# Kernel tuning notes

Measured on AMD Instinct MI355X. Metric: run time of the kernel, lower is better.

Reference implementation:

```python
import jax, jax.numpy as jnp
import numpy as np

N_NODES = 100000
N_EDGES = 3200000
F_IN = 128
H = 32
C = 8


def _graph_conv(x, src, dst, ew, W_rel, b_rel, W_root):
    # PyG GraphConv: sum-aggregate edge_weight * x[src] into dst, then
    # lin_rel(agg) + lin_root(x). lin_root has no bias.
    msg = x[src] * ew[:, None]                                  # [E, F]
    agg = jax.ops.segment_sum(msg, dst, num_segments=N_NODES)   # [N, F]
    return agg @ W_rel.T + b_rel + x @ W_root.T


def setup_inputs() -> dict:
    key = jax.random.key(0)
    ks = jax.random.split(key, 12)
    x = jax.random.normal(ks[0], (N_NODES, F_IN), dtype=jnp.float32)
    edge_index = jax.random.randint(ks[1], (2, N_EDGES), 0, N_NODES, dtype=jnp.int32)
    edge_weights = jax.random.uniform(ks[2], (N_EDGES,), dtype=jnp.float32)
    s = lambda fan_in: 1.0 / np.sqrt(fan_in)
    W1_rel = jax.random.uniform(ks[3], (H, F_IN), minval=-s(F_IN), maxval=s(F_IN), dtype=jnp.float32)
    b1 = jax.random.uniform(ks[4], (H,), minval=-s(F_IN), maxval=s(F_IN), dtype=jnp.float32)
    W1_root = jax.random.uniform(ks[5], (H, F_IN), minval=-s(F_IN), maxval=s(F_IN), dtype=jnp.float32)
    W2_rel = jax.random.uniform(ks[6], (H, H), minval=-s(H), maxval=s(H), dtype=jnp.float32)
    b2 = jax.random.uniform(ks[7], (H,), minval=-s(H), maxval=s(H), dtype=jnp.float32)
    W2_root = jax.random.uniform(ks[8], (H, H), minval=-s(H), maxval=s(H), dtype=jnp.float32)
    W3_rel = jax.random.uniform(ks[9], (C, H), minval=-s(H), maxval=s(H), dtype=jnp.float32)
    b3 = jax.random.uniform(ks[10], (C,), minval=-s(H), maxval=s(H), dtype=jnp.float32)
    W3_root = jax.random.uniform(ks[11], (C, H), minval=-s(H), maxval=s(H), dtype=jnp.float32)
    return {"x": x, "edge_index": edge_index, "edge_weights": edge_weights,
            "W1_rel": W1_rel, "b1": b1, "W1_root": W1_root,
            "W2_rel": W2_rel, "b2": b2, "W2_root": W2_root,
            "W3_rel": W3_rel, "b3": b3, "W3_root": W3_root}


def reference(x, edge_index, edge_weights,
              W1_rel, b1, W1_root, W2_rel, b2, W2_root, W3_rel, b3, W3_root):
    src, dst = edge_index[0], edge_index[1]
    h = _graph_conv(x, src, dst, edge_weights, W1_rel, b1, W1_root)
    h = jax.nn.leaky_relu(h, negative_slope=0.01)
    # dropout is identity in eval mode
    h = _graph_conv(h, src, dst, edge_weights, W2_rel, b2, W2_root)
    h = jax.nn.leaky_relu(h, negative_slope=0.01)
    out = _graph_conv(h, src, dst, edge_weights, W3_rel, b3, W3_root)
    return out
```

## Files before the change

### kernel.cpp

```cpp
#include <hip/hip_runtime.h>

#define NN 100000
#define NE 3200000
#define FIN 128
#define HD 32
#define CD 8
#define NPB 256
#define NBUCK ((NN + NPB - 1) / NPB)
#define CHUNK_B 8192

typedef unsigned int uint;

__device__ __forceinline__ float lrelu(float v) { return v > 0.f ? v : 0.01f * v; }
__device__ __forceinline__ uint bf16rne(float x) {
    uint u = __float_as_uint(x);
    return (u + 0x7FFFu + ((u >> 16) & 1u)) >> 16;
}
__device__ __forceinline__ uint pack2(float a, float b) {
    return bf16rne(a) | (bf16rne(b) << 16);
}
__device__ __forceinline__ float lo16(uint v) { return __uint_as_float(v << 16); }
__device__ __forceinline__ float hi16(uint v) { return __uint_as_float(v & 0xFFFF0000u); }


__global__ __launch_bounds__(256) void k_proj128(
    const float* __restrict__ x, const float* __restrict__ Wrel,
    const float* __restrict__ Wroot, const float* __restrict__ b,
    uint* __restrict__ pB, float* __restrict__ R)
{
    __shared__ float Wt[FIN][64];
    for (int idx = threadIdx.x; idx < FIN * 64; idx += 256) {
        int k = idx >> 6, j = idx & 63;
        Wt[k][j] = (j < HD) ? Wrel[j * FIN + k] : Wroot[(j - HD) * FIN + k];
    }
    __syncthreads();
    int n = blockIdx.x * 256 + threadIdx.x;
    if (n >= NN) return;

    float accP[HD], accR[HD];
#pragma unroll
    for (int j = 0; j < HD; ++j) { accP[j] = 0.f; accR[j] = 0.f; }

    const float4* x4 = (const float4*)(x + (size_t)n * FIN);
#pragma unroll 2
    for (int k4 = 0; k4 < FIN / 4; ++k4) {
        float4 xv = x4[k4];
        float xs[4] = {xv.x, xv.y, xv.z, xv.w};
#pragma unroll
        for (int kk = 0; kk < 4; ++kk) {
            float xk = xs[kk];
            int k = k4 * 4 + kk;
#pragma unroll
            for (int j = 0; j < HD; ++j) {
                accP[j] += xk * Wt[k][j];
                accR[j] += xk * Wt[k][j + HD];
            }
        }
    }
    uint4* pp = (uint4*)(pB + (size_t)n * 16);
#pragma unroll
    for (int q = 0; q < 4; ++q)
        pp[q] = make_uint4(pack2(accP[8*q+0], accP[8*q+1]), pack2(accP[8*q+2], accP[8*q+3]),
                           pack2(accP[8*q+4], accP[8*q+5]), pack2(accP[8*q+6], accP[8*q+7]));
    float4* rr = (float4*)(R + (size_t)n * HD);
#pragma unroll
    for (int q = 0; q < HD / 4; ++q)
        rr[q] = make_float4(accR[4*q+0] + b[4*q+0], accR[4*q+1] + b[4*q+1],
                            accR[4*q+2] + b[4*q+2], accR[4*q+3] + b[4*q+3]);
}

__global__ __launch_bounds__(256) void k_mid(
    const float* __restrict__ G, const float* R_in,
    const float* __restrict__ Wrel, const float* __restrict__ Wroot,
    const float* __restrict__ b,
    uint* __restrict__ pB, float* R_out)
{
    __shared__ float Ws[HD][64];
    for (int idx = threadIdx.x; idx < HD * 64; idx += 256) {
        int k = idx >> 6, j = idx & 63;
        Ws[k][j] = (j < HD) ? Wrel[j * HD + k] : Wroot[(j - HD) * HD + k];
    }
    __syncthreads();
    int n = blockIdx.x * 256 + threadIdx.x;
    if (n >= NN) return;

    float h[HD];
    const float4* av = (const float4*)(G + (size_t)n * HD);
    const float4* rv = (const float4*)(R_in + (size_t)n * HD);
#pragma unroll
    for (int q = 0; q < HD / 4; ++q) {
        float4 a = av[q], r_ = rv[q];
        h[4*q+0] = lrelu(a.x + r_.x);
        h[4*q+1] = lrelu(a.y + r_.y);
        h[4*q+2] = lrelu(a.z + r_.z);
        h[4*q+3] = lrelu(a.w + r_.w);
    }
    float accP[HD], accR[HD];
#pragma unroll
    for (int j = 0; j < HD; ++j) { accP[j] = 0.f; accR[j] = 0.f; }
#pragma unroll 4
    for (int k = 0; k < HD; ++k) {
        float hk = h[k];
#pragma unroll
        for (int j = 0; j < HD; ++j) {
            accP[j] += hk * Ws[k][j];
            accR[j] += hk * Ws[k][j + HD];
        }
    }
    uint4* pp = (uint4*)(pB + (size_t)n * 16);
#pragma unroll
    for (int q = 0; q < 4; ++q)
        pp[q] = make_uint4(pack2(accP[8*q+0], accP[8*q+1]), pack2(accP[8*q+2], accP[8*q+3]),
                           pack2(accP[8*q+4], accP[8*q+5]), pack2(accP[8*q+6], accP[8*q+7]));
    float4* rr = (float4*)(R_out + (size_t)n * HD);
#pragma unroll
    for (int q = 0; q < HD / 4; ++q)
        rr[q] = make_float4(accR[4*q+0] + b[4*q+0], accR[4*q+1] + b[4*q+1],
                            accR[4*q+2] + b[4*q+2], accR[4*q+3] + b[4*q+3]);
}

__global__ __launch_bounds__(256) void k_last(
    const float* __restrict__ G, const float* __restrict__ R,
    const float* __restrict__ Wrel, const float* __restrict__ Wroot,
    const float* __restrict__ b,
    uint* __restrict__ p3B, float* __restrict__ out)
{
    __shared__ float Ws[HD][16];
    for (int idx = threadIdx.x; idx < HD * 16; idx += 256) {
        int k = idx >> 4, j = idx & 15;
        Ws[k][j] = (j < CD) ? Wrel[j * HD + k] : Wroot[(j - CD) * HD + k];
    }
    __syncthreads();
    int n = blockIdx.x * 256 + threadIdx.x;
    if (n >= NN) return;

    float h[HD];
    const float4* av = (const float4*)(G + (size_t)n * HD);
    const float4* rv = (const float4*)(R + (size_t)n * HD);
#pragma unroll
    for (int q = 0; q < HD / 4; ++q) {
        float4 a = av[q], r_ = rv[q];
        h[4*q+0] = lrelu(a.x + r_.x);
        h[4*q+1] = lrelu(a.y + r_.y);
        h[4*q+2] = lrelu(a.z + r_.z);
        h[4*q+3] = lrelu(a.w + r_.w);
    }
    float accP[CD], accR[CD];
#pragma unroll
    for (int j = 0; j < CD; ++j) { accP[j] = 0.f; accR[j] = 0.f; }
#pragma unroll
    for (int k = 0; k < HD; ++k) {
        float hk = h[k];
#pragma unroll
        for (int j = 0; j < CD; ++j) {
            accP[j] += hk * Ws[k][j];
            accR[j] += hk * Ws[k][j + CD];
        }
    }
    uint4* pp = (uint4*)(p3B + (size_t)n * 4);
    pp[0] = make_uint4(pack2(accP[0], accP[1]), pack2(accP[2], accP[3]),
                       pack2(accP[4], accP[5]), pack2(accP[6], accP[7]));
    float4* oo = (float4*)(out + (size_t)n * CD);
    oo[0] = make_float4(accR[0] + b[0], accR[1] + b[1], accR[2] + b[2], accR[3] + b[3]);
    oo[1] = make_float4(accR[4] + b[4], accR[5] + b[5], accR[6] + b[6], accR[7] + b[7]);
}


__global__ __launch_bounds__(256) void k_bhist(
    const int* __restrict__ dst, int* __restrict__ bcnt)
{
    __shared__ int lc[NBUCK];
    int t = threadIdx.x;
    for (int i = t; i < NBUCK; i += 256) lc[i] = 0;
    __syncthreads();
    for (int e = blockIdx.x * 256 + t; e < NE; e += gridDim.x * 256)
        atomicAdd(&lc[dst[e] >> 8], 1);
    __syncthreads();
    for (int i = t; i < NBUCK; i += 256) {
        int c = lc[i];
        if (c) atomicAdd(&bcnt[i], c);
    }
}

__global__ __launch_bounds__(512) void k_bscan(
    const int* __restrict__ bcnt, int* __restrict__ bbase, int* __restrict__ bcur)
{
    __shared__ int s[512];
    int t = threadIdx.x;
    s[t] = (t < NBUCK) ? bcnt[t] : 0;
    __syncthreads();
    for (int off = 1; off < 512; off <<= 1) {
        int a = (t >= off) ? s[t - off] : 0;
        __syncthreads();
        s[t] += a;
        __syncthreads();
    }
    int excl = t ? s[t - 1] : 0;
    if (t < NBUCK) { bbase[t] = excl; bcur[t] = excl; }
    if (t == 0) bbase[NBUCK] = NE;
}

__global__ __launch_bounds__(256) void k_bscatter(
    const int* __restrict__ src, const int* __restrict__ dst, const float* __restrict__ ew,
    int* __restrict__ bcur, int2* __restrict__ tmp)
{
    __shared__ int lc[NBUCK];
    int t = threadIdx.x;
    for (int i = t; i < NBUCK; i += 256) lc[i] = 0;
    __syncthreads();
    int base = blockIdx.x * CHUNK_B;
#pragma unroll 4
    for (int k = 0; k < CHUNK_B / 256; ++k) {
        int e = base + k * 256 + t;
        if (e < NE) atomicAdd(&lc[dst[e] >> 8], 1);
    }
    __syncthreads();
    for (int b = t; b < NBUCK; b += 256) {
        int c = lc[b];
        lc[b] = c ? atomicAdd(&bcur[b], c) : 0;
    }
    __syncthreads();
#pragma unroll 4
    for (int k = 0; k < CHUNK_B / 256; ++k) {
        int e = base + k * 256 + t;
        if (e < NE) {
            int d = dst[e];
            int pos = atomicAdd(&lc[d >> 8], 1);
            tmp[pos] = make_int2(src[e] | ((d & 255) << 17), __float_as_int(ew[e]));
        }
    }
}

__global__ __launch_bounds__(256) void k_bsort(
    const int* __restrict__ bbase, const int2* __restrict__ tmp,
    int2* __restrict__ epack, int* __restrict__ rowstart)
{
    int b = blockIdx.x, t = threadIdx.x;
    int lo = bbase[b], hi = bbase[b + 1], cnt = hi - lo;
    __shared__ int hist[NPB];
    __shared__ int sc[NPB];
    __shared__ int cur[NPB];
    hist[t] = 0;
    __syncthreads();
    for (int i = t; i < cnt; i += 256)
        atomicAdd(&hist[(tmp[lo + i].x >> 17) & 255], 1);
    __syncthreads();
    sc[t] = hist[t];
    __syncthreads();
    for (int off = 1; off < 256; off <<= 1) {
        int a = (t >= off) ? sc[t - off] : 0;
        __syncthreads();
        sc[t] += a;
        __syncthreads();
    }
    int excl = t ? sc[t - 1] : 0;
    int node = (b << 8) + t;
    if (node < NN) rowstart[node] = lo + excl;
    if (b == 0 && t == 0) rowstart[NN] = NE;
    cur[t] = lo + excl;
    __syncthreads();
    for (int i = t; i < cnt; i += 256) {
        int2 v = tmp[lo + i];
        int l = (v.x >> 17) & 255;
        int pos = atomicAdd(&cur[l], 1);
        epack[pos] = make_int2(v.x & 0x1FFFF, v.y);
    }
}


__global__ __launch_bounds__(256) void k_gather32(
    const int* __restrict__ rowstart, const int2* __restrict__ epack,
    const uint* __restrict__ pB, float* __restrict__ G)
{
    int wid = (blockIdx.x * 256 + threadIdx.x) >> 6;
    if (wid >= NN) return;
    int lane = threadIdx.x & 63;
    int q = lane >> 4, f2 = lane & 15;
    int rs = rowstart[wid], re = rowstart[wid + 1];

    float a0 = 0.f, a1 = 0.f, b0 = 0.f, b1 = 0.f;
    int e = rs + q;
    for (; e + 4 < re; e += 8) {
        int2 p0 = epack[e];
        int2 p1 = epack[e + 4];
        uint v0 = pB[((size_t)p0.x << 4) + f2];
        uint v1 = pB[((size_t)p1.x << 4) + f2];
        float w0 = __int_as_float(p0.y), w1 = __int_as_float(p1.y);
        a0 += lo16(v0) * w0; a1 += hi16(v0) * w0;
        b0 += lo16(v1) * w1; b1 += hi16(v1) * w1;
    }
    for (; e < re; e += 4) {
        int2 p0 = epack[e];
        uint v0 = pB[((size_t)p0.x << 4) + f2];
        float w0 = __int_as_float(p0.y);
        a0 += lo16(v0) * w0; a1 += hi16(v0) * w0;
    }
    a0 += b0; a1 += b1;
    a0 += __shfl_xor(a0, 16); a1 += __shfl_xor(a1, 16);
    a0 += __shfl_xor(a0, 32); a1 += __shfl_xor(a1, 32);
    if (lane < 16) {
        float2* g2 = (float2*)(G + (size_t)wid * HD + 2 * f2);
        *g2 = make_float2(a0, a1);
    }
}

__global__ __launch_bounds__(256) void k_gather8(
    const int* __restrict__ rowstart, const int2* __restrict__ epack,
    const uint* __restrict__ p3B, float* __restrict__ out)
{
    int wid = (blockIdx.x * 256 + threadIdx.x) >> 6;
    if (wid >= NN) return;
    int lane = threadIdx.x & 63;
    int q = lane >> 2, f2 = lane & 3;
    int rs = rowstart[wid], re = rowstart[wid + 1];

    float a0 = 0.f, a1 = 0.f, b0 = 0.f, b1 = 0.f;
    int e = rs + q;
    for (; e + 16 < re; e += 32) {
        int2 p0 = epack[e];
        int2 p1 = epack[e + 16];
        uint v0 = p3B[((size_t)p0.x << 2) + f2];
        uint v1 = p3B[((size_t)p1.x << 2) + f2];
        float w0 = __int_as_float(p0.y), w1 = __int_as_float(p1.y);
        a0 += lo16(v0) * w0; a1 += hi16(v0) * w0;
        b0 += lo16(v1) * w1; b1 += hi16(v1) * w1;
    }
    for (; e < re; e += 16) {
        int2 p0 = epack[e];
        uint v0 = p3B[((size_t)p0.x << 2) + f2];
        float w0 = __int_as_float(p0.y);
        a0 += lo16(v0) * w0; a1 += hi16(v0) * w0;
    }
    a0 += b0; a1 += b1;
    a0 += __shfl_xor(a0, 4);  a1 += __shfl_xor(a1, 4);
    a0 += __shfl_xor(a0, 8);  a1 += __shfl_xor(a1, 8);
    a0 += __shfl_xor(a0, 16); a1 += __shfl_xor(a1, 16);
    a0 += __shfl_xor(a0, 32); a1 += __shfl_xor(a1, 32);
    if (lane < 4) {
        float2* o2 = (float2*)(out + (size_t)wid * CD + 2 * f2);
        float2 t = *o2;
        t.x += a0; t.y += a1;
        *o2 = t;
    }
}


extern "C" void kernel_launch(void* const* d_in, const int* in_sizes, int n_in,
                              void* d_out, int out_size, void* d_ws, size_t ws_size,
                              hipStream_t stream)
{
    const float* x      = (const float*)d_in[0];
    const int*   ei     = (const int*)d_in[1];
    const float* ew     = (const float*)d_in[2];
    const float* W1rel  = (const float*)d_in[3];
    const float* b1     = (const float*)d_in[4];
    const float* W1root = (const float*)d_in[5];
    const float* W2rel  = (const float*)d_in[6];
    const float* b2     = (const float*)d_in[7];
    const float* W2root = (const float*)d_in[8];
    const float* W3rel  = (const float*)d_in[9];
    const float* b3     = (const float*)d_in[10];
    const float* W3root = (const float*)d_in[11];
    float* out = (float*)d_out;

    const int* src = ei;
    const int* dst = ei + NE;

    char* ws = (char*)d_ws;
    int2*  epack    = (int2*)ws;   ws += (size_t)NE * sizeof(int2);
    char*  unionA   = ws;          ws += (size_t)NE * sizeof(int2);
    uint*  pB       = (uint*)ws;   ws += (size_t)NN * 16 * 4;
    uint*  p3B      = (uint*)ws;   ws += (size_t)NN * 4 * 4;
    int*   rowstart = (int*)ws;    ws += (size_t)(NN + 1) * 4;
    int*   bcnt     = (int*)ws;    ws += (size_t)NBUCK * 4;
    int*   bbase    = (int*)ws;    ws += (size_t)(NBUCK + 1) * 4;
    int*   bcur     = (int*)ws;

    int2*  tmp = (int2*)unionA;
    float* G   = (float*)unionA;
    float* R   = G + (size_t)NN * HD;

    const int nodeBlocks = (NN + 255) / 256;
    const int waveBlocks = (NN + 3) / 4;
    const int scatBlocks = (NE + CHUNK_B - 1) / CHUNK_B;

    hipMemsetAsync(bcnt, 0, (size_t)NBUCK * 4, stream);
    k_bhist<<<512, 256, 0, stream>>>(dst, bcnt);
    k_bscan<<<1, 512, 0, stream>>>(bcnt, bbase, bcur);
    k_bscatter<<<scatBlocks, 256, 0, stream>>>(src, dst, ew, bcur, tmp);
    k_bsort<<<NBUCK, 256, 0, stream>>>(bbase, tmp, epack, rowstart);

    k_proj128<<<nodeBlocks, 256, 0, stream>>>(x, W1rel, W1root, b1, pB, R);
    k_gather32<<<waveBlocks, 256, 0, stream>>>(rowstart, epack, pB, G);
    k_mid<<<nodeBlocks, 256, 0, stream>>>(G, R, W2rel, W2root, b2, pB, R);
    k_gather32<<<waveBlocks, 256, 0, stream>>>(rowstart, epack, pB, G);
    k_last<<<nodeBlocks, 256, 0, stream>>>(G, R, W3rel, W3root, b3, p3B, out);
    k_gather8<<<waveBlocks, 256, 0, stream>>>(rowstart, epack, p3B, out);
}
```

Before: 484.9 us.

## Fuse per-node projections into gather kernels and vectorize edge bucketing loads

Merges the mid and last per-node projection kernels into the gather kernels. Each wave aggregates its node, applies leaky-relu with the root term, stores the hidden vector in shared memory and computes the next layer's projections per lane. This removes two kernel launches and the global round trip of the aggregated G buffer, but needs separate pB1/pB2 buffers and a block-wide sync after the gather. The histogram and scatter kernels are also changed to read int4/float4 vectors with 512-thread blocks, the sort kernel moves to 512 threads, and the gather loop is unrolled by three instead of two.

```diff
diff --git a/kernel.cpp b/kernel.cpp
--- a/kernel.cpp
+++ b/kernel.cpp
@@ -2,6 +2,7 @@
 
 #define NN 100000
 #define NE 3200000
+#define NE4 (NE / 4)
 #define FIN 128
 #define HD 32
 #define CD 8
@@ -69,114 +70,24 @@
                             accR[4*q+2] + b[4*q+2], accR[4*q+3] + b[4*q+3]);
 }
 
-__global__ __launch_bounds__(256) void k_mid(
-    const float* __restrict__ G, const float* R_in,
-    const float* __restrict__ Wrel, const float* __restrict__ Wroot,
-    const float* __restrict__ b,
-    uint* __restrict__ pB, float* R_out)
-{
-    __shared__ float Ws[HD][64];
-    for (int idx = threadIdx.x; idx < HD * 64; idx += 256) {
-        int k = idx >> 6, j = idx & 63;
-        Ws[k][j] = (j < HD) ? Wrel[j * HD + k] : Wroot[(j - HD) * HD + k];
-    }
-    __syncthreads();
-    int n = blockIdx.x * 256 + threadIdx.x;
-    if (n >= NN) return;
-
-    float h[HD];
-    const float4* av = (const float4*)(G + (size_t)n * HD);
-    const float4* rv = (const float4*)(R_in + (size_t)n * HD);
-#pragma unroll
-    for (int q = 0; q < HD / 4; ++q) {
-        float4 a = av[q], r_ = rv[q];
-        h[4*q+0] = lrelu(a.x + r_.x);
-        h[4*q+1] = lrelu(a.y + r_.y);
-        h[4*q+2] = lrelu(a.z + r_.z);
-        h[4*q+3] = lrelu(a.w + r_.w);
-    }
-    float accP[HD], accR[HD];
-#pragma unroll
-    for (int j = 0; j < HD; ++j) { accP[j] = 0.f; accR[j] = 0.f; }
-#pragma unroll 4
-    for (int k = 0; k < HD; ++k) {
-        float hk = h[k];
-#pragma unroll
-        for (int j = 0; j < HD; ++j) {
-            accP[j] += hk * Ws[k][j];
-            accR[j] += hk * Ws[k][j + HD];
-        }
-    }
-    uint4* pp = (uint4*)(pB + (size_t)n * 16);
-#pragma unroll
-    for (int q = 0; q < 4; ++q)
-        pp[q] = make_uint4(pack2(accP[8*q+0], accP[8*q+1]), pack2(accP[8*q+2], accP[8*q+3]),
-                           pack2(accP[8*q+4], accP[8*q+5]), pack2(accP[8*q+6], accP[8*q+7]));
-    float4* rr = (float4*)(R_out + (size_t)n * HD);
-#pragma unroll
-    for (int q = 0; q < HD / 4; ++q)
-        rr[q] = make_float4(accR[4*q+0] + b[4*q+0], accR[4*q+1] + b[4*q+1],
-                            accR[4*q+2] + b[4*q+2], accR[4*q+3] + b[4*q+3]);
-}
-
-__global__ __launch_bounds__(256) void k_last(
-    const float* __restrict__ G, const float* __restrict__ R,
-    const float* __restrict__ Wrel, const float* __restrict__ Wroot,
-    const float* __restrict__ b,
-    uint* __restrict__ p3B, float* __restrict__ out)
-{
-    __shared__ float Ws[HD][16];
-    for (int idx = threadIdx.x; idx < HD * 16; idx += 256) {
-        int k = idx >> 4, j = idx & 15;
-        Ws[k][j] = (j < CD) ? Wrel[j * HD + k] : Wroot[(j - CD) * HD + k];
-    }
-    __syncthreads();
-    int n = blockIdx.x * 256 + threadIdx.x;
-    if (n >= NN) return;
-
-    float h[HD];
-    const float4* av = (const float4*)(G + (size_t)n * HD);
-    const float4* rv = (const float4*)(R + (size_t)n * HD);
-#pragma unroll
-    for (int q = 0; q < HD / 4; ++q) {
-        float4 a = av[q], r_ = rv[q];
-        h[4*q+0] = lrelu(a.x + r_.x);
-        h[4*q+1] = lrelu(a.y + r_.y);
-        h[4*q+2] = lrelu(a.z + r_.z);
-        h[4*q+3] = lrelu(a.w + r_.w);
-    }
-    float accP[CD], accR[CD];
-#pragma unroll
-    for (int j = 0; j < CD; ++j) { accP[j] = 0.f; accR[j] = 0.f; }
-#pragma unroll
-    for (int k = 0; k < HD; ++k) {
-        float hk = h[k];
-#pragma unroll
-        for (int j = 0; j < CD; ++j) {
-            accP[j] += hk * Ws[k][j];
-            accR[j] += hk * Ws[k][j + CD];
-        }
-    }
-    uint4* pp = (uint4*)(p3B + (size_t)n * 4);
-    pp[0] = make_uint4(pack2(accP[0], accP[1]), pack2(accP[2], accP[3]),
-                       pack2(accP[4], accP[5]), pack2(accP[6], accP[7]));
-    float4* oo = (float4*)(out + (size_t)n * CD);
-    oo[0] = make_float4(accR[0] + b[0], accR[1] + b[1], accR[2] + b[2], accR[3] + b[3]);
-    oo[1] = make_float4(accR[4] + b[4], accR[5] + b[5], accR[6] + b[6], accR[7] + b[7]);
-}
-
-
-__global__ __launch_bounds__(256) void k_bhist(
+
+__global__ __launch_bounds__(512) void k_bhist(
     const int* __restrict__ dst, int* __restrict__ bcnt)
 {
     __shared__ int lc[NBUCK];
     int t = threadIdx.x;
-    for (int i = t; i < NBUCK; i += 256) lc[i] = 0;
-    __syncthreads();
-    for (int e = blockIdx.x * 256 + t; e < NE; e += gridDim.x * 256)
-        atomicAdd(&lc[dst[e] >> 8], 1);
-    __syncthreads();
-    for (int i = t; i < NBUCK; i += 256) {
+    for (int i = t; i < NBUCK; i += 512) lc[i] = 0;
+    __syncthreads();
+    const int4* dst4 = (const int4*)dst;
+    for (int i4 = blockIdx.x * 512 + t; i4 < NE4; i4 += gridDim.x * 512) {
+        int4 d = dst4[i4];
+        atomicAdd(&lc[d.x >> 8], 1);
+        atomicAdd(&lc[d.y >> 8], 1);
+        atomicAdd(&lc[d.z >> 8], 1);
+        atomicAdd(&lc[d.w >> 8], 1);
+    }
+    __syncthreads();
+    for (int i = t; i < NBUCK; i += 512) {
         int c = lc[i];
         if (c) atomicAdd(&bcnt[i], c);
     }
@@ -200,38 +111,52 @@
     if (t == 0) bbase[NBUCK] = NE;
 }
 
-__global__ __launch_bounds__(256) void k_bscatter(
+__global__ __launch_bounds__(512) void k_bscatter(
     const int* __restrict__ src, const int* __restrict__ dst, const float* __restrict__ ew,
     int* __restrict__ bcur, int2* __restrict__ tmp)
 {
     __shared__ int lc[NBUCK];
     int t = threadIdx.x;
-    for (int i = t; i < NBUCK; i += 256) lc[i] = 0;
-    __syncthreads();
-    int base = blockIdx.x * CHUNK_B;
-#pragma unroll 4
-    for (int k = 0; k < CHUNK_B / 256; ++k) {
-        int e = base + k * 256 + t;
-        if (e < NE) atomicAdd(&lc[dst[e] >> 8], 1);
-    }
-    __syncthreads();
-    for (int b = t; b < NBUCK; b += 256) {
+    for (int i = t; i < NBUCK; i += 512) lc[i] = 0;
+    __syncthreads();
+    const int4* dst4 = (const int4*)dst;
+    const int4* src4 = (const int4*)src;
+    const float4* ew4 = (const float4*)ew;
+    int base4 = blockIdx.x * (CHUNK_B / 4);
+#pragma unroll
+    for (int k = 0; k < CHUNK_B / 4 / 512; ++k) {
+        int i4 = base4 + k * 512 + t;
+        if (i4 < NE4) {
+            int4 d = dst4[i4];
+            atomicAdd(&lc[d.x >> 8], 1);
+            atomicAdd(&lc[d.y >> 8], 1);
+            atomicAdd(&lc[d.z >> 8], 1);
+            atomicAdd(&lc[d.w >> 8], 1);
+        }
+    }
+    __syncthreads();
+    for (int b = t; b < NBUCK; b += 512) {
         int c = lc[b];
         lc[b] = c ? atomicAdd(&bcur[b], c) : 0;
     }
     __syncthreads();
-#pragma unroll 4
-    for (int k = 0; k < CHUNK_B / 256; ++k) {
-        int e = base + k * 256 + t;
-        if (e < NE) {
-            int d = dst[e];
-            int pos = atomicAdd(&lc[d >> 8], 1);
-            tmp[pos] = make_int2(src[e] | ((d & 255) << 17), __float_as_int(ew[e]));
+#pragma unroll
+    for (int k = 0; k < CHUNK_B / 4 / 512; ++k) {
+        int i4 = base4 + k * 512 + t;
+        if (i4 < NE4) {
+            int4 d = dst4[i4];
+            int4 s = src4[i4];
+            float4 w = ew4[i4];
+            int pos;
+            pos = atomicAdd(&lc[d.x >> 8], 1); tmp[pos] = make_int2(s.x | ((d.x & 255) << 17), __float_as_int(w.x));
+            pos = atomicAdd(&lc[d.y >> 8], 1); tmp[pos] = make_int2(s.y | ((d.y & 255) << 17), __float_as_int(w.y));
+            pos = atomicAdd(&lc[d.z >> 8], 1); tmp[pos] = make_int2(s.z | ((d.z & 255) << 17), __float_as_int(w.z));
+            pos = atomicAdd(&lc[d.w >> 8], 1); tmp[pos] = make_int2(s.w | ((d.w & 255) << 17), __float_as_int(w.w));
         }
     }
 }
 
-__global__ __launch_bounds__(256) void k_bsort(
+__global__ __launch_bounds__(512) void k_bsort(
     const int* __restrict__ bbase, const int2* __restrict__ tmp,
     int2* __restrict__ epack, int* __restrict__ rowstart)
 {
@@ -240,26 +165,28 @@
     __shared__ int hist[NPB];
     __shared__ int sc[NPB];
     __shared__ int cur[NPB];
-    hist[t] = 0;
-    __syncthreads();
-    for (int i = t; i < cnt; i += 256)
+    if (t < NPB) hist[t] = 0;
+    __syncthreads();
+    for (int i = t; i < cnt; i += 512)
         atomicAdd(&hist[(tmp[lo + i].x >> 17) & 255], 1);
     __syncthreads();
-    sc[t] = hist[t];
-    __syncthreads();
-    for (int off = 1; off < 256; off <<= 1) {
-        int a = (t >= off) ? sc[t - off] : 0;
+    if (t < NPB) sc[t] = hist[t];
+    __syncthreads();
+    for (int off = 1; off < NPB; off <<= 1) {
+        int a = (t < NPB && t >= off) ? sc[t - off] : 0;
         __syncthreads();
-        sc[t] += a;
+        if (t < NPB) sc[t] += a;
         __syncthreads();
     }
-    int excl = t ? sc[t - 1] : 0;
-    int node = (b << 8) + t;
-    if (node < NN) rowstart[node] = lo + excl;
+    if (t < NPB) {
+        int excl = t ? sc[t - 1] : 0;
+        int node = (b << 8) + t;
+        if (node < NN) rowstart[node] = lo + excl;
+        cur[t] = lo + excl;
+    }
     if (b == 0 && t == 0) rowstart[NN] = NE;
-    cur[t] = lo + excl;
-    __syncthreads();
-    for (int i = t; i < cnt; i += 256) {
+    __syncthreads();
+    for (int i = t; i < cnt; i += 512) {
         int2 v = tmp[lo + i];
         int l = (v.x >> 17) & 255;
         int pos = atomicAdd(&cur[l], 1);
@@ -268,39 +195,125 @@
 }
 
 
-__global__ __launch_bounds__(256) void k_gather32(
+__global__ __launch_bounds__(256) void k_gatherMid(
     const int* __restrict__ rowstart, const int2* __restrict__ epack,
-    const uint* __restrict__ pB, float* __restrict__ G)
-{
+    const uint* __restrict__ pB1, float* R,
+    const float* __restrict__ Wrel, const float* __restrict__ Wroot,
+    const float* __restrict__ b2, uint* __restrict__ pB2)
+{
+    __shared__ float Ws[HD][64];
+    __shared__ float hS[4][HD];
+    for (int idx = threadIdx.x; idx < HD * 64; idx += 256) {
+        int k = idx >> 6, j = idx & 63;
+        Ws[k][j] = (j < HD) ? Wrel[j * HD + k] : Wroot[(j - HD) * HD + k];
+    }
     int wid = (blockIdx.x * 256 + threadIdx.x) >> 6;
-    if (wid >= NN) return;
     int lane = threadIdx.x & 63;
+    int w = threadIdx.x >> 6;
     int q = lane >> 4, f2 = lane & 15;
     int rs = rowstart[wid], re = rowstart[wid + 1];
 
-    float a0 = 0.f, a1 = 0.f, b0 = 0.f, b1 = 0.f;
+    float a0 = 0.f, a1 = 0.f, c0 = 0.f, c1 = 0.f, d0 = 0.f, d1 = 0.f;
     int e = rs + q;
-    for (; e + 4 < re; e += 8) {
+    for (; e + 8 < re; e += 12) {
         int2 p0 = epack[e];
         int2 p1 = epack[e + 4];
-        uint v0 = pB[((size_t)p0.x << 4) + f2];
-        uint v1 = pB[((size_t)p1.x << 4) + f2];
-        float w0 = __int_as_float(p0.y), w1 = __int_as_float(p1.y);
-        a0 += lo16(v0) * w0; a1 += hi16(v0) * w0;
-        b0 += lo16(v1) * w1; b1 += hi16(v1) * w1;
+        int2 p2 = epack[e + 8];
+        uint v0 = pB1[((size_t)p0.x << 4) + f2];
+        uint v1 = pB1[((size_t)p1.x << 4) + f2];
+        uint v2 = pB1[((size_t)p2.x << 4) + f2];
+        float w0 = __int_as_float(p0.y), w1 = __int_as_float(p1.y), w2 = __int_as_float(p2.y);
+        a0 += lo16(v0) * w0; a1 += hi16(v0) * w0;
+        c0 += lo16(v1) * w1; c1 += hi16(v1) * w1;
+        d0 += lo16(v2) * w2; d1 += hi16(v2) * w2;
     }
     for (; e < re; e += 4) {
         int2 p0 = epack[e];
-        uint v0 = pB[((size_t)p0.x << 4) + f2];
+        uint v0 = pB1[((size_t)p0.x << 4) + f2];
         float w0 = __int_as_float(p0.y);
         a0 += lo16(v0) * w0; a1 += hi16(v0) * w0;
     }
-    a0 += b0; a1 += b1;
+    a0 += c0 + d0; a1 += c1 + d1;
     a0 += __shfl_xor(a0, 16); a1 += __shfl_xor(a1, 16);
     a0 += __shfl_xor(a0, 32); a1 += __shfl_xor(a1, 32);
     if (lane < 16) {
-        float2* g2 = (float2*)(G + (size_t)wid * HD + 2 * f2);
-        *g2 = make_float2(a0, a1);
+        float2 rv = *(const float2*)(R + (size_t)wid * HD + 2 * f2);
+        float2 hv = make_float2(lrelu(a0 + rv.x), lrelu(a1 + rv.y));
+        *(float2*)&hS[w][2 * f2] = hv;
+    }
+    __syncthreads();
+
+    int j = lane;
+    float acc = 0.f;
+#pragma unroll 8
+    for (int k = 0; k < HD; ++k) acc += hS[w][k] * Ws[k][j];
+    float other = __shfl_xor(acc, 1);
+    if (j < HD) {
+        if (!(j & 1)) pB2[(size_t)wid * 16 + (j >> 1)] = pack2(acc, other);
+    } else {
+        R[(size_t)wid * HD + (j - HD)] = acc + b2[j - HD];
+    }
+}
+
+__global__ __launch_bounds__(256) void k_gatherLast(
+    const int* __restrict__ rowstart, const int2* __restrict__ epack,
+    const uint* __restrict__ pB2, const float* __restrict__ R,
+    const float* __restrict__ Wrel, const float* __restrict__ Wroot,
+    const float* __restrict__ b3, uint* __restrict__ p3B, float* __restrict__ out)
+{
+    __shared__ float Ws[HD][16];
+    __shared__ float hS[4][HD];
+    for (int idx = threadIdx.x; idx < HD * 16; idx += 256) {
+        int k = idx >> 4, j = idx & 15;
+        Ws[k][j] = (j < CD) ? Wrel[j * HD + k] : Wroot[(j - CD) * HD + k];
+    }
+    int wid = (blockIdx.x * 256 + threadIdx.x) >> 6;
+    int lane = threadIdx.x & 63;
+    int w = threadIdx.x >> 6;
+    int q = lane >> 4, f2 = lane & 15;
+    int rs = rowstart[wid], re = rowstart[wid + 1];
+
+    float a0 = 0.f, a1 = 0.f, c0 = 0.f, c1 = 0.f, d0 = 0.f, d1 = 0.f;
+    int e = rs + q;
+    for (; e + 8 < re; e += 12) {
+        int2 p0 = epack[e];
+        int2 p1 = epack[e + 4];
+        int2 p2 = epack[e + 8];
+        uint v0 = pB2[((size_t)p0.x << 4) + f2];
+        uint v1 = pB2[((size_t)p1.x << 4) + f2];
+        uint v2 = pB2[((size_t)p2.x << 4) + f2];
+        float w0 = __int_as_float(p0.y), w1 = __int_as_float(p1.y), w2 = __int_as_float(p2.y);
+        a0 += lo16(v0) * w0; a1 += hi16(v0) * w0;
+        c0 += lo16(v1) * w1; c1 += hi16(v1) * w1;
+        d0 += lo16(v2) * w2; d1 += hi16(v2) * w2;
+    }
+    for (; e < re; e += 4) {
+        int2 p0 = epack[e];
+        uint v0 = pB2[((size_t)p0.x << 4) + f2];
+        float w0 = __int_as_float(p0.y);
+        a0 += lo16(v0) * w0; a1 += hi16(v0) * w0;
+    }
+    a0 += c0 + d0; a1 += c1 + d1;
+    a0 += __shfl_xor(a0, 16); a1 += __shfl_xor(a1, 16);
+    a0 += __shfl_xor(a0, 32); a1 += __shfl_xor(a1, 32);
+    if (lane < 16) {
+        float2 rv = *(const float2*)(R + (size_t)wid * HD + 2 * f2);
+        float2 hv = make_float2(lrelu(a0 + rv.x), lrelu(a1 + rv.y));
+        *(float2*)&hS[w][2 * f2] = hv;
+    }
+    __syncthreads();
+
+    if (lane < 16) {
+        int j = lane;
+        float acc = 0.f;
+#pragma unroll 8
+        for (int k = 0; k < HD; ++k) acc += hS[w][k] * Ws[k][j];
+        float other = __shfl_xor(acc, 1);
+        if (j < CD) {
+            if (!(j & 1)) p3B[(size_t)wid * 4 + (j >> 1)] = pack2(acc, other);
+        } else {
+            out[(size_t)wid * CD + (j - CD)] = acc + b3[j - CD];
+        }
     }
 }
 
@@ -368,32 +381,28 @@
 
     char* ws = (char*)d_ws;
     int2*  epack    = (int2*)ws;   ws += (size_t)NE * sizeof(int2);
-    char*  unionA   = ws;          ws += (size_t)NE * sizeof(int2);
-    uint*  pB       = (uint*)ws;   ws += (size_t)NN * 16 * 4;
+    int2*  tmp      = (int2*)ws;   ws += (size_t)NE * sizeof(int2);
+    float* R        = (float*)ws;  ws += (size_t)NN * HD * 4;
+    uint*  pB1      = (uint*)ws;   ws += (size_t)NN * 16 * 4;
+    uint*  pB2      = (uint*)ws;   ws += (size_t)NN * 16 * 4;
     uint*  p3B      = (uint*)ws;   ws += (size_t)NN * 4 * 4;
     int*   rowstart = (int*)ws;    ws += (size_t)(NN + 1) * 4;
     int*   bcnt     = (int*)ws;    ws += (size_t)NBUCK * 4;
     int*   bbase    = (int*)ws;    ws += (size_t)(NBUCK + 1) * 4;
     int*   bcur     = (int*)ws;
 
-    int2*  tmp = (int2*)unionA;
-    float* G   = (float*)unionA;
-    float* R   = G + (size_t)NN * HD;
-
     const int nodeBlocks = (NN + 255) / 256;
     const int waveBlocks = (NN + 3) / 4;
     const int scatBlocks = (NE + CHUNK_B - 1) / CHUNK_B;
 
     hipMemsetAsync(bcnt, 0, (size_t)NBUCK * 4, stream);
-    k_bhist<<<512, 256, 0, stream>>>(dst, bcnt);
+    k_bhist<<<512, 512, 0, stream>>>(dst, bcnt);
     k_bscan<<<1, 512, 0, stream>>>(bcnt, bbase, bcur);
-    k_bscatter<<<scatBlocks, 256, 0, stream>>>(src, dst, ew, bcur, tmp);
-    k_bsort<<<NBUCK, 256, 0, stream>>>(bbase, tmp, epack, rowstart);
-
-    k_proj128<<<nodeBlocks, 256, 0, stream>>>(x, W1rel, W1root, b1, pB, R);
-    k_gather32<<<waveBlocks, 256, 0, stream>>>(rowstart, epack, pB, G);
-    k_mid<<<nodeBlocks, 256, 0, stream>>>(G, R, W2rel, W2root, b2, pB, R);
-    k_gather32<<<waveBlocks, 256, 0, stream>>>(rowstart, epack, pB, G);
-    k_last<<<nodeBlocks, 256, 0, stream>>>(G, R, W3rel, W3root, b3, p3B, out);
+    k_bscatter<<<scatBlocks, 512, 0, stream>>>(src, dst, ew, bcur, tmp);
+    k_bsort<<<NBUCK, 512, 0, stream>>>(bbase, tmp, epack, rowstart);
+
+    k_proj128<<<nodeBlocks, 256, 0, stream>>>(x, W1rel, W1root, b1, pB1, R);
+    k_gatherMid<<<waveBlocks, 256, 0, stream>>>(rowstart, epack, pB1, R, W2rel, W2root, b2, pB2);
+    k_gatherLast<<<waveBlocks, 256, 0, stream>>>(rowstart, epack, pB2, R, W3rel, W3root, b3, p3B, out);
     k_gather8<<<waveBlocks, 256, 0, stream>>>(rowstart, epack, p3B, out);
 }
```

New measurement: 525.5 us. 1.08x slower.

## Locally sort bucket scatter in shared memory for coalesced writes; widen sort kernels

Applied to the files above, without the earlier changes.

The bucket scatter kernel now builds a per-chunk permutation in shared memory. It scans the local histogram so that edges of the same bucket are written to contiguous global positions, instead of each edge being scattered on its own through a shared atomic. The histogram kernel reads dst four at a time as int4, and the three sort-phase kernels move to 512-thread blocks. The aim is more coalesced global writes and fewer memory transactions in the CSR build. The cost is extra shared-memory use, an added 512-wide scan, and a second read of dst per chunk.

```diff
diff --git a/kernel.cpp b/kernel.cpp
--- a/kernel.cpp
+++ b/kernel.cpp
@@ -2,6 +2,7 @@
 
 #define NN 100000
 #define NE 3200000
+#define NE4 (NE / 4)
 #define FIN 128
 #define HD 32
 #define CD 8
@@ -10,6 +11,7 @@
 #define CHUNK_B 8192
 
 typedef unsigned int uint;
+typedef unsigned short ushort;
 
 __device__ __forceinline__ float lrelu(float v) { return v > 0.f ? v : 0.01f * v; }
 __device__ __forceinline__ uint bf16rne(float x) {
@@ -68,6 +70,7 @@
         rr[q] = make_float4(accR[4*q+0] + b[4*q+0], accR[4*q+1] + b[4*q+1],
                             accR[4*q+2] + b[4*q+2], accR[4*q+3] + b[4*q+3]);
 }
+
 
 __global__ __launch_bounds__(256) void k_mid(
     const float* __restrict__ G, const float* R_in,
@@ -166,17 +169,23 @@
 }
 
 
-__global__ __launch_bounds__(256) void k_bhist(
+__global__ __launch_bounds__(512) void k_bhist(
     const int* __restrict__ dst, int* __restrict__ bcnt)
 {
     __shared__ int lc[NBUCK];
     int t = threadIdx.x;
-    for (int i = t; i < NBUCK; i += 256) lc[i] = 0;
-    __syncthreads();
-    for (int e = blockIdx.x * 256 + t; e < NE; e += gridDim.x * 256)
-        atomicAdd(&lc[dst[e] >> 8], 1);
-    __syncthreads();
-    for (int i = t; i < NBUCK; i += 256) {
+    for (int i = t; i < NBUCK; i += 512) lc[i] = 0;
+    __syncthreads();
+    const int4* dst4 = (const int4*)dst;
+    for (int i4 = blockIdx.x * 512 + t; i4 < NE4; i4 += gridDim.x * 512) {
+        int4 d = dst4[i4];
+        atomicAdd(&lc[d.x >> 8], 1);
+        atomicAdd(&lc[d.y >> 8], 1);
+        atomicAdd(&lc[d.z >> 8], 1);
+        atomicAdd(&lc[d.w >> 8], 1);
+    }
+    __syncthreads();
+    for (int i = t; i < NBUCK; i += 512) {
         int c = lc[i];
         if (c) atomicAdd(&bcnt[i], c);
     }
@@ -200,38 +209,54 @@
     if (t == 0) bbase[NBUCK] = NE;
 }
 
-__global__ __launch_bounds__(256) void k_bscatter(
+__global__ __launch_bounds__(512) void k_bscatter(
     const int* __restrict__ src, const int* __restrict__ dst, const float* __restrict__ ew,
     int* __restrict__ bcur, int2* __restrict__ tmp)
 {
-    __shared__ int lc[NBUCK];
+    __shared__ int hist[NBUCK];
+    __shared__ int s[512];
+    __shared__ int off[NBUCK];
+    __shared__ int cur[NBUCK];
+    __shared__ ushort perm[CHUNK_B];
     int t = threadIdx.x;
-    for (int i = t; i < NBUCK; i += 256) lc[i] = 0;
-    __syncthreads();
     int base = blockIdx.x * CHUNK_B;
-#pragma unroll 4
-    for (int k = 0; k < CHUNK_B / 256; ++k) {
-        int e = base + k * 256 + t;
-        if (e < NE) atomicAdd(&lc[dst[e] >> 8], 1);
-    }
-    __syncthreads();
-    for (int b = t; b < NBUCK; b += 256) {
-        int c = lc[b];
-        lc[b] = c ? atomicAdd(&bcur[b], c) : 0;
-    }
-    __syncthreads();
-#pragma unroll 4
-    for (int k = 0; k < CHUNK_B / 256; ++k) {
-        int e = base + k * 256 + t;
-        if (e < NE) {
-            int d = dst[e];
-            int pos = atomicAdd(&lc[d >> 8], 1);
-            tmp[pos] = make_int2(src[e] | ((d & 255) << 17), __float_as_int(ew[e]));
-        }
-    }
-}
-
-__global__ __launch_bounds__(256) void k_bsort(
+    int cnt = min(CHUNK_B, NE - base);
+
+    for (int i = t; i < NBUCK; i += 512) hist[i] = 0;
+    __syncthreads();
+    for (int i = t; i < cnt; i += 512)
+        atomicAdd(&hist[dst[base + i] >> 8], 1);
+    __syncthreads();
+    s[t] = (t < NBUCK) ? hist[t] : 0;
+    __syncthreads();
+    for (int o = 1; o < 512; o <<= 1) {
+        int a = (t >= o) ? s[t - o] : 0;
+        __syncthreads();
+        s[t] += a;
+        __syncthreads();
+    }
+    if (t < NBUCK) {
+        int excl = t ? s[t - 1] : 0;
+        int c = hist[t];
+        int g = c ? atomicAdd(&bcur[t], c) : 0;
+        off[t] = g - excl;
+        cur[t] = excl;
+    }
+    __syncthreads();
+    for (int i = t; i < cnt; i += 512) {
+        int b = dst[base + i] >> 8;
+        int r = atomicAdd(&cur[b], 1);
+        perm[r] = (ushort)i;
+    }
+    __syncthreads();
+    for (int i = t; i < cnt; i += 512) {
+        int e = base + (int)perm[i];
+        int d = dst[e];
+        tmp[off[d >> 8] + i] = make_int2(src[e] | ((d & 255) << 17), __float_as_int(ew[e]));
+    }
+}
+
+__global__ __launch_bounds__(512) void k_bsort(
     const int* __restrict__ bbase, const int2* __restrict__ tmp,
     int2* __restrict__ epack, int* __restrict__ rowstart)
 {
@@ -240,26 +265,28 @@
     __shared__ int hist[NPB];
     __shared__ int sc[NPB];
     __shared__ int cur[NPB];
-    hist[t] = 0;
-    __syncthreads();
-    for (int i = t; i < cnt; i += 256)
+    if (t < NPB) hist[t] = 0;
+    __syncthreads();
+    for (int i = t; i < cnt; i += 512)
         atomicAdd(&hist[(tmp[lo + i].x >> 17) & 255], 1);
     __syncthreads();
-    sc[t] = hist[t];
-    __syncthreads();
-    for (int off = 1; off < 256; off <<= 1) {
-        int a = (t >= off) ? sc[t - off] : 0;
-        __syncthreads();
-        sc[t] += a;
-        __syncthreads();
-    }
-    int excl = t ? sc[t - 1] : 0;
-    int node = (b << 8) + t;
-    if (node < NN) rowstart[node] = lo + excl;
+    if (t < NPB) sc[t] = hist[t];
+    __syncthreads();
+    for (int off = 1; off < NPB; off <<= 1) {
+        int a = (t < NPB && t >= off) ? sc[t - off] : 0;
+        __syncthreads();
+        if (t < NPB) sc[t] += a;
+        __syncthreads();
+    }
+    if (t < NPB) {
+        int excl = t ? sc[t - 1] : 0;
+        int node = (b << 8) + t;
+        if (node < NN) rowstart[node] = lo + excl;
+        cur[t] = lo + excl;
+    }
     if (b == 0 && t == 0) rowstart[NN] = NE;
-    cur[t] = lo + excl;
-    __syncthreads();
-    for (int i = t; i < cnt; i += 256) {
+    __syncthreads();
+    for (int i = t; i < cnt; i += 512) {
         int2 v = tmp[lo + i];
         int l = (v.x >> 17) & 255;
         int pos = atomicAdd(&cur[l], 1);
@@ -385,10 +412,10 @@
     const int scatBlocks = (NE + CHUNK_B - 1) / CHUNK_B;
 
     hipMemsetAsync(bcnt, 0, (size_t)NBUCK * 4, stream);
-    k_bhist<<<512, 256, 0, stream>>>(dst, bcnt);
+    k_bhist<<<512, 512, 0, stream>>>(dst, bcnt);
     k_bscan<<<1, 512, 0, stream>>>(bcnt, bbase, bcur);
-    k_bscatter<<<scatBlocks, 256, 0, stream>>>(src, dst, ew, bcur, tmp);
-    k_bsort<<<NBUCK, 256, 0, stream>>>(bbase, tmp, epack, rowstart);
+    k_bscatter<<<scatBlocks, 512, 0, stream>>>(src, dst, ew, bcur, tmp);
+    k_bsort<<<NBUCK, 512, 0, stream>>>(bbase, tmp, epack, rowstart);
 
     k_proj128<<<nodeBlocks, 256, 0, stream>>>(x, W1rel, W1root, b1, pB, R);
     k_gather32<<<waveBlocks, 256, 0, stream>>>(rowstart, epack, pB, G);
```

Result: faster. 462.0 us (-4.7%).
